# Optimization experiments

Hardware: AMD Instinct MI355X
Metric: run time of the kernel (lower is better)

Reference implementation:

```python
import jax, jax.numpy as jnp
import numpy as np

N = 8192      # nodes
E = 16384     # edges
G = 512       # graphs
IN = 235      # node feature dim (input_dim)
H = 64        # hidden_dim
ED = 52       # edge feature dim


def setup_inputs() -> dict:
    key = jax.random.key(0)
    ks = jax.random.split(key, 24)
    s = lambda fan_in: 1.0 / np.sqrt(fan_in)
    inp = {}
    inp["x"] = jax.random.normal(ks[0], (N, IN), dtype=jnp.float32)
    inp["edge_index"] = jax.random.randint(ks[1], (2, E), 0, N)
    inp["edge_attr"] = jax.random.uniform(ks[2], (E, ED), dtype=jnp.float32)
    inp["batch"] = jnp.sort(jax.random.randint(ks[3], (N,), 0, G))
    # EdgeModel (nn of nnconv1): Linear(52,128) -> Linear(128, 235*64)
    inp["W1"] = jax.random.normal(ks[4], (128, ED), dtype=jnp.float32) * s(ED)
    inp["b1"] = jnp.zeros((128,), jnp.float32)
    inp["W2"] = jax.random.normal(ks[5], (IN * H, 128), dtype=jnp.float32) * s(128)
    inp["b2"] = jnp.zeros((IN * H,), jnp.float32)
    # NNConv root weight and bias
    inp["root"] = jax.random.normal(ks[6], (IN, H), dtype=jnp.float32) * s(IN)
    inp["conv_b"] = jnp.zeros((H,), jnp.float32)
    # MLP head
    inp["fw1"] = jax.random.normal(ks[7], (128, H), dtype=jnp.float32) * s(H)
    inp["fb1"] = jnp.zeros((128,), jnp.float32)
    inp["fw2"] = jax.random.normal(ks[8], (256, 128), dtype=jnp.float32) * s(128)
    inp["fb2"] = jnp.zeros((256,), jnp.float32)
    inp["fw3"] = jax.random.normal(ks[9], (128, 256), dtype=jnp.float32) * s(256)
    inp["fb3"] = jnp.zeros((128,), jnp.float32)
    inp["fw4"] = jax.random.normal(ks[10], (1, 128), dtype=jnp.float32) * s(128)
    inp["fb4"] = jnp.zeros((1,), jnp.float32)
    return inp


def reference(x, edge_index, edge_attr, batch, W1, b1, W2, b2, root, conv_b,
              fw1, fb1, fw2, fb2, fw3, fb3, fw4, fb4):
    src, dst = edge_index[0], edge_index[1]
    # edge MLP -> per-edge weight matrices [E, IN, H]
    h = edge_attr @ W1.T + b1
    w = (h @ W2.T + b2).reshape(E, IN, H)
    # gather source node feats, per-edge matmul, scatter-add to destinations
    msg = jnp.einsum('ei,eih->eh', x[src], w)          # [E, H]
    agg = jax.ops.segment_sum(msg, dst, num_segments=N)  # [N, H]
    out = jax.nn.relu(agg + x @ root + conv_b)           # NNConv + ReLU
    # global mean pool per graph
    summ = jax.ops.segment_sum(out, batch, num_segments=G)
    cnt = jax.ops.segment_sum(jnp.ones((N, 1), out.dtype), batch, num_segments=G)
    pooled = summ / jnp.maximum(cnt, 1.0)                # [G, H]
    # dense MLP head
    y = jax.nn.relu(pooled @ fw1.T + fb1)
    y = jax.nn.relu(y @ fw2.T + fb2)
    y = jax.nn.relu(y @ fw3.T + fb3)
    return y @ fw4.T + fb4                               # [G, 1]
```

## Files before the change

kernel.cpp:

```cpp
#include <hip/hip_runtime.h>
#include <hip/hip_bf16.h>
#include <stdint.h>

#define N_NODES 8192
#define N_EDGES 16384
#define N_GRAPHS 512
#define IN_DIM 235
#define H_DIM 64
#define ED_DIM 52
#define HID1 128
#define KP 256
#define NB 3328
#define NBP 3584

#define BT_BLOCKS 940
#define EXT_BLOCKS 128
#define ZERO_BLOCKS 16
#define PREP_GRID (BT_BLOCKS + EXT_BLOCKS + ZERO_BLOCKS + N_NODES)

typedef __bf16 bf16x8 __attribute__((ext_vector_type(8)));
typedef float f32x4 __attribute__((ext_vector_type(4)));

static __device__ inline unsigned short f2bf(float f) {
    union { float f; unsigned u; } v; v.f = f;
    unsigned r = v.u + 0x7FFFu + ((v.u >> 16) & 1u);
    return (unsigned short)(r >> 16);
}

__global__ __launch_bounds__(256) void k_prep(const float* __restrict__ x,
                                              const float* __restrict__ W1,
                                              const float* __restrict__ W2,
                                              const float* __restrict__ b1,
                                              const float* __restrict__ b2,
                                              const float* __restrict__ root,
                                              unsigned short* __restrict__ A,
                                              unsigned short* __restrict__ Bt) {
    __shared__ float w1s[ED_DIM * 132];
    __shared__ float w2s[16 * 132];
    const int bx = blockIdx.x;
    const int t = threadIdx.x;

    if (bx < BT_BLOCKS) {
        const int i = bx >> 2;
        const int by = bx & 3;
        for (int j = t; j < ED_DIM * HID1; j += 256) {
            const int k = j / ED_DIM, d = j - k * ED_DIM;
            w1s[d * 132 + k] = W1[j];
        }
        const float* w2src = W2 + ((size_t)i * 64 + by * 16) * HID1;
        for (int j = t; j < 16 * HID1; j += 256) w2s[(j >> 7) * 132 + (j & 127)] = w2src[j];
        __syncthreads();
        const int hh = t & 15, dq = t >> 4;
        const float4* w2v = (const float4*)&w2s[hh * 132];
        #pragma unroll
        for (int m = 0; m < 4; ++m) {
            const int d = dq + m * 16;
            if (d >= ED_DIM) break;
            const float4* w1v = (const float4*)&w1s[d * 132];
            float acc = 0.f;
            #pragma unroll
            for (int k4 = 0; k4 < HID1 / 4; ++k4) {
                const float4 a = w1v[k4], b = w2v[k4];
                acc += a.x * b.x + a.y * b.y + a.z * b.z + a.w * b.w;
            }
            const int p = (by * 16 + hh) * ED_DIM + d;
            Bt[(size_t)p * KP + i] = f2bf(acc);
        }
    } else if (bx < BT_BLOCKS + EXT_BLOCKS) {
        const int j = bx - BT_BLOCKS;
        const int i = t;
        if (i < IN_DIM) {
            float v;
            if (j < 64) {
                v = root[i * H_DIM + j];
            } else {
                const int jj = i * H_DIM + (j - 64);
                float acc = b2[jj];
                const float* w = W2 + (size_t)jj * HID1;
                #pragma unroll 8
                for (int k = 0; k < HID1; ++k) acc += w[k] * b1[k];
                v = acc;
            }
            Bt[(size_t)(NB + j) * KP + i] = f2bf(v);
        }
    } else if (bx < BT_BLOCKS + EXT_BLOCKS + ZERO_BLOCKS) {
        const int z = bx - BT_BLOCKS - EXT_BLOCKS;
        const int R1 = NBP * 21;
        const int TOT = R1 + 128 * IN_DIM;
        for (int idx = z * 256 + t; idx < TOT; idx += ZERO_BLOCKS * 256) {
            size_t off;
            if (idx < R1) {
                const int r = idx / 21, c = IN_DIM + idx - (idx / 21) * 21;
                off = (size_t)r * KP + c;
            } else {
                const int k = idx - R1;
                const int r = 3456 + k / IN_DIM, c = k - (k / IN_DIM) * IN_DIM;
                off = (size_t)r * KP + c;
            }
            Bt[off] = 0;
        }
    } else {
        const int j = (bx - BT_BLOCKS - EXT_BLOCKS - ZERO_BLOCKS) * 256 + t;
        const int n = j >> 8, i = j & 255;
        A[j] = (i < IN_DIM) ? f2bf(x[n * IN_DIM + i]) : (unsigned short)0;
    }
}

__global__ __launch_bounds__(1024, 4) void k_gemm(const unsigned short* __restrict__ A,
                                                  const unsigned short* __restrict__ Bt,
                                                  unsigned short* __restrict__ P,
                                                  float* __restrict__ agg,
                                                  float* __restrict__ xb2,
                                                  const float* __restrict__ conv_b) {
    __shared__ unsigned short As[2 * 256 * 32];
    __shared__ unsigned short Bs[2 * 256 * 32];
    const int t = threadIdx.x;
    const int lin = blockIdx.x;
    const int xcd = lin & 7, bi = lin >> 3;
    const int mt = (bi / 14) * 8 + xcd;
    const int nt = bi % 14;
    const int m0 = mt * 256, n0 = nt * 256;
    const int wid = t >> 6, lane = t & 63;
    const int wm = wid & 3;
    const int wn = wid >> 2;
    const int q = lane >> 4, r16 = lane & 15;

    f32x4 acc[4][4] = {};

    auto stage = [&](int k0, int buf) {
        const int idx = t;
        const int row = idx >> 2;
        const int lgrp = ((idx & 3) ^ ((row >> 1) & 3)) * 8;
        const unsigned short* ga = &A[(size_t)(m0 + row) * KP + k0 + lgrp];
        const unsigned short* gb = &Bt[(size_t)(n0 + row) * KP + k0 + lgrp];
        char* la = (char*)As + buf * 16384 + wid * 1024;
        char* lb = (char*)Bs + buf * 16384 + wid * 1024;
        __builtin_amdgcn_global_load_lds(
            (const __attribute__((address_space(1))) unsigned int*)ga,
            (__attribute__((address_space(3))) unsigned int*)la, 16, 0, 0);
        __builtin_amdgcn_global_load_lds(
            (const __attribute__((address_space(1))) unsigned int*)gb,
            (__attribute__((address_space(3))) unsigned int*)lb, 16, 0, 0);
    };

    stage(0, 0);
    const int pcq = (q ^ ((r16 >> 1) & 3)) * 8;
    #pragma unroll
    for (int it = 0; it < 8; ++it) {
        __syncthreads();
        if (it < 7) stage((it + 1) * 32, (it + 1) & 1);
        const int bo = (it & 1) * 8192;
        bf16x8 af[4], bfr[4];
        #pragma unroll
        for (int mi = 0; mi < 4; ++mi)
            af[mi] = *(const bf16x8*)(&As[bo + (wm * 64 + mi * 16 + r16) * 32 + pcq]);
        #pragma unroll
        for (int ni = 0; ni < 4; ++ni)
            bfr[ni] = *(const bf16x8*)(&Bs[bo + (wn * 64 + ni * 16 + r16) * 32 + pcq]);
        #pragma unroll
        for (int mi = 0; mi < 4; ++mi)
            #pragma unroll
            for (int ni = 0; ni < 4; ++ni)
                acc[mi][ni] = __builtin_amdgcn_mfma_f32_16x16x32_bf16(
                    bfr[ni], af[mi], acc[mi][ni], 0, 0, 0);
    }

    if (n0 < NB) {
        #pragma unroll
        for (int mi = 0; mi < 4; ++mi)
            #pragma unroll
            for (int ni = 0; ni < 4; ++ni) {
                const int row = m0 + wm * 64 + mi * 16 + r16;
                const int col = n0 + wn * 64 + ni * 16 + q * 4;
                union { unsigned short us[4]; uint2 u2; } pk;
                #pragma unroll
                for (int rr = 0; rr < 4; ++rr) pk.us[rr] = f2bf(acc[mi][ni][rr]);
                *(uint2*)(&P[(size_t)row * NB + col]) = pk.u2;
            }
    } else if (wn < 2) {
        #pragma unroll
        for (int mi = 0; mi < 4; ++mi)
            #pragma unroll
            for (int ni = 0; ni < 4; ++ni) {
                const int row = m0 + wm * 64 + mi * 16 + r16;
                const int cl = ni * 16 + q * 4;
                if (wn == 0) {
                    const float4 cb = *(const float4*)&conv_b[cl];
                    float4 v;
                    v.x = acc[mi][ni][0] + cb.x; v.y = acc[mi][ni][1] + cb.y;
                    v.z = acc[mi][ni][2] + cb.z; v.w = acc[mi][ni][3] + cb.w;
                    *(float4*)(&agg[row * H_DIM + cl]) = v;
                } else {
                    float4 v;
                    v.x = acc[mi][ni][0]; v.y = acc[mi][ni][1];
                    v.z = acc[mi][ni][2]; v.w = acc[mi][ni][3];
                    *(float4*)(&xb2[row * H_DIM + cl]) = v;
                }
            }
    }
}

__global__ __launch_bounds__(256) void k_edge(const int* __restrict__ ei,
                                              const float* __restrict__ ea,
                                              const unsigned short* __restrict__ P,
                                              const float* __restrict__ xb2,
                                              float* __restrict__ agg) {
    const int e = (blockIdx.x * 256 + threadIdx.x) >> 6;
    const int h = threadIdx.x & 63;
    if (e >= N_EDGES) return;
    const int s = ei[e], dst = ei[N_EDGES + e];
    const uint2* Pr = (const uint2*)(P + (size_t)s * NB + h * ED_DIM);
    const float4* ev = (const float4*)(ea + (size_t)e * ED_DIM);

    uint2 pv[13];
    #pragma unroll
    for (int j = 0; j < 13; ++j) pv[j] = Pr[j];
    float4 eav[13];
    #pragma unroll
    for (int j = 0; j < 13; ++j) eav[j] = ev[j];

    float acc = xb2[s * H_DIM + h];
    #pragma unroll
    for (int j = 0; j < 13; ++j) {
        union { unsigned u; float f; } a0, a1, b0, b1;
        a0.u = pv[j].x << 16; a1.u = pv[j].x & 0xffff0000u;
        b0.u = pv[j].y << 16; b1.u = pv[j].y & 0xffff0000u;
        acc += eav[j].x * a0.f + eav[j].y * a1.f
             + eav[j].z * b0.f + eav[j].w * b1.f;
    }
    atomicAdd(&agg[dst * H_DIM + h], acc);
}

__global__ __launch_bounds__(256) void k_tail(const float* __restrict__ agg,
                                              const int* __restrict__ batch,
                                              const float* __restrict__ fw1, const float* __restrict__ fb1,
                                              const float* __restrict__ fw2, const float* __restrict__ fb2,
                                              const float* __restrict__ fw3, const float* __restrict__ fb3,
                                              const float* __restrict__ fw4, const float* __restrict__ fb4,
                                              float* __restrict__ out) {
    __shared__ float red[256];
    __shared__ float sp[64], s1[128], s2[256], s3[128];
    const int g = blockIdx.x, t = threadIdx.x;

    int lo = 0, hi = N_NODES;
    while (lo < hi) { const int mid = (lo + hi) >> 1; if (batch[mid] < g) lo = mid + 1; else hi = mid; }
    const int start = lo;
    hi = N_NODES;
    while (lo < hi) { const int mid = (lo + hi) >> 1; if (batch[mid] <= g) lo = mid + 1; else hi = mid; }
    const int end = lo;
    const float inv = 1.0f / fmaxf((float)(end - start), 1.0f);

    float a = 0.f;
    for (int n = start + (t >> 6); n < end; n += 4)
        a += fmaxf(agg[n * H_DIM + (t & 63)], 0.f);
    red[t] = a;
    __syncthreads();
    if (t < 64) sp[t] = (red[t] + red[t + 64] + red[t + 128] + red[t + 192]) * inv;
    __syncthreads();

    if (t < 128) {
        float acc = fb1[t];
        const float* w = fw1 + t * 64;
        #pragma unroll 8
        for (int k = 0; k < 64; ++k) acc += sp[k] * w[k];
        s1[t] = fmaxf(acc, 0.f);
    }
    __syncthreads();
    {
        float acc = fb2[t];
        const float* w = fw2 + t * 128;
        #pragma unroll 8
        for (int k = 0; k < 128; ++k) acc += s1[k] * w[k];
        s2[t] = fmaxf(acc, 0.f);
    }
    __syncthreads();
    if (t < 128) {
        float acc = fb3[t];
        const float* w = fw3 + t * 256;
        #pragma unroll 8
        for (int k = 0; k < 256; ++k) acc += s2[k] * w[k];
        s3[t] = fmaxf(acc, 0.f);
    }
    __syncthreads();
    if (t < 64) {
        float p = s3[t] * fw4[t] + s3[t + 64] * fw4[t + 64];
        #pragma unroll
        for (int off = 32; off > 0; off >>= 1) p += __shfl_down(p, off);
        if (t == 0) out[g] = p + fb4[0];
    }
}

extern "C" void kernel_launch(void* const* d_in, const int* in_sizes, int n_in,
                              void* d_out, int out_size, void* d_ws, size_t ws_size,
                              hipStream_t stream) {
    const float* x      = (const float*)d_in[0];
    const int*   ei     = (const int*)d_in[1];
    const float* ea     = (const float*)d_in[2];
    const int*   batch  = (const int*)d_in[3];
    const float* W1     = (const float*)d_in[4];
    const float* b1     = (const float*)d_in[5];
    const float* W2     = (const float*)d_in[6];
    const float* b2     = (const float*)d_in[7];
    const float* root   = (const float*)d_in[8];
    const float* conv_b = (const float*)d_in[9];
    const float* fw1 = (const float*)d_in[10]; const float* fb1 = (const float*)d_in[11];
    const float* fw2 = (const float*)d_in[12]; const float* fb2 = (const float*)d_in[13];
    const float* fw3 = (const float*)d_in[14]; const float* fb3 = (const float*)d_in[15];
    const float* fw4 = (const float*)d_in[16]; const float* fb4 = (const float*)d_in[17];
    float* out = (float*)d_out;

    char* ws = (char*)d_ws;
    unsigned short* A   = (unsigned short*)(ws);
    unsigned short* Bt  = (unsigned short*)(ws + 4194304);
    unsigned short* P   = (unsigned short*)(ws + 6029312);
    float* agg  = (float*)(ws + 60555264);
    float* xb2  = (float*)(ws + 62652416);

    k_prep<<<dim3(PREP_GRID), dim3(256), 0, stream>>>(x, W1, W2, b1, b2, root, A, Bt);
    k_gemm<<<dim3(448), dim3(1024), 0, stream>>>(A, Bt, P, agg, xb2, conv_b);
    k_edge<<<dim3(N_EDGES / 4), dim3(256), 0, stream>>>(ei, ea, P, xb2, agg);
    k_tail<<<dim3(N_GRAPHS), dim3(256), 0, stream>>>(agg, batch, fw1, fb1, fw2, fb2, fw3, fb3, fw4, fb4, out);
}
```

Before: 188.3 us.

## Bucket edges by source node to reuse per-node P rows in edge kernel

Adds a bucketing pass that groups edge ids by source node with atomic counters, plus a small overflow list for nodes with more than 16 outgoing edges. The edge kernel now runs one wavefront per source node: it loads that node's projected P row once into registers and loops over the node's edges, instead of re-reading the row for every edge. This is meant to cut the redundant P gather traffic. In exchange it adds a kernel launch and per-node load imbalance. Edges past the overflow cap would be silently dropped.

```diff
diff --git a/kernel.cpp b/kernel.cpp
--- a/kernel.cpp
+++ b/kernel.cpp
@@ -18,6 +18,9 @@
 #define ZERO_BLOCKS 16
 #define PREP_GRID (BT_BLOCKS + EXT_BLOCKS + ZERO_BLOCKS + N_NODES)
 
+#define BUCKET_CAP 16
+#define OVF_CAP 255
+
 typedef __bf16 bf16x8 __attribute__((ext_vector_type(8)));
 typedef float f32x4 __attribute__((ext_vector_type(4)));
 
@@ -34,7 +37,9 @@
                                               const float* __restrict__ b2,
                                               const float* __restrict__ root,
                                               unsigned short* __restrict__ A,
-                                              unsigned short* __restrict__ Bt) {
+                                              unsigned short* __restrict__ Bt,
+                                              int* __restrict__ cnt,
+                                              int* __restrict__ ovf) {
     __shared__ float w1s[ED_DIM * 132];
     __shared__ float w2s[16 * 132];
     const int bx = blockIdx.x;
@@ -99,10 +104,29 @@
             }
             Bt[off] = 0;
         }
+        for (int idx = z * 256 + t; idx < N_NODES + OVF_CAP + 1; idx += ZERO_BLOCKS * 256) {
+            if (idx < N_NODES) cnt[idx] = 0;
+            else ovf[idx - N_NODES] = 0;
+        }
     } else {
         const int j = (bx - BT_BLOCKS - EXT_BLOCKS - ZERO_BLOCKS) * 256 + t;
         const int n = j >> 8, i = j & 255;
         A[j] = (i < IN_DIM) ? f2bf(x[n * IN_DIM + i]) : (unsigned short)0;
+    }
+}
+
+__global__ __launch_bounds__(256) void k_bucket(const int* __restrict__ ei,
+                                                int* __restrict__ cnt,
+                                                int* __restrict__ bucket,
+                                                int* __restrict__ ovf) {
+    const int e = blockIdx.x * 256 + threadIdx.x;
+    if (e >= N_EDGES) return;
+    const int s = ei[e];
+    const int slot = atomicAdd(&cnt[s], 1);
+    if (slot < BUCKET_CAP) bucket[s * BUCKET_CAP + slot] = e;
+    else {
+        const int p = atomicAdd(&ovf[0], 1);
+        if (p < OVF_CAP) ovf[1 + p] = e;
     }
 }
 
@@ -200,35 +224,61 @@
     }
 }
 
-__global__ __launch_bounds__(256) void k_edge(const int* __restrict__ ei,
-                                              const float* __restrict__ ea,
-                                              const unsigned short* __restrict__ P,
-                                              const float* __restrict__ xb2,
-                                              float* __restrict__ agg) {
-    const int e = (blockIdx.x * 256 + threadIdx.x) >> 6;
-    const int h = threadIdx.x & 63;
-    if (e >= N_EDGES) return;
-    const int s = ei[e], dst = ei[N_EDGES + e];
-    const uint2* Pr = (const uint2*)(P + (size_t)s * NB + h * ED_DIM);
-    const float4* ev = (const float4*)(ea + (size_t)e * ED_DIM);
-
-    uint2 pv[13];
-    #pragma unroll
-    for (int j = 0; j < 13; ++j) pv[j] = Pr[j];
-    float4 eav[13];
-    #pragma unroll
-    for (int j = 0; j < 13; ++j) eav[j] = ev[j];
-
-    float acc = xb2[s * H_DIM + h];
-    #pragma unroll
-    for (int j = 0; j < 13; ++j) {
-        union { unsigned u; float f; } a0, a1, b0, b1;
-        a0.u = pv[j].x << 16; a1.u = pv[j].x & 0xffff0000u;
-        b0.u = pv[j].y << 16; b1.u = pv[j].y & 0xffff0000u;
-        acc += eav[j].x * a0.f + eav[j].y * a1.f
-             + eav[j].z * b0.f + eav[j].w * b1.f;
-    }
-    atomicAdd(&agg[dst * H_DIM + h], acc);
+__global__ __launch_bounds__(256) void k_edge2(const int* __restrict__ ei,
+                                               const float* __restrict__ ea,
+                                               const unsigned short* __restrict__ P,
+                                               const float* __restrict__ xb2,
+                                               float* __restrict__ agg,
+                                               const int* __restrict__ cnt,
+                                               const int* __restrict__ bucket,
+                                               const int* __restrict__ ovf) {
+    const int wv = threadIdx.x >> 6, h = threadIdx.x & 63;
+    if (blockIdx.x < N_NODES / 4) {
+        const int n = blockIdx.x * 4 + wv;
+        int deg = cnt[n];
+        if (deg <= 0) return;
+        if (deg > BUCKET_CAP) deg = BUCKET_CAP;
+        const uint2* Pr = (const uint2*)(P + (size_t)n * NB + h * ED_DIM);
+        uint2 pv[13];
+        #pragma unroll
+        for (int j = 0; j < 13; ++j) pv[j] = Pr[j];
+        const float xb = xb2[n * H_DIM + h];
+        for (int j = 0; j < deg; ++j) {
+            const int e = bucket[n * BUCKET_CAP + j];
+            const int dst = ei[N_EDGES + e];
+            const float4* ev = (const float4*)(ea + (size_t)e * ED_DIM);
+            float acc = xb;
+            #pragma unroll
+            for (int k = 0; k < 13; ++k) {
+                const float4 ee = ev[k];
+                union { unsigned u; float f; } a0, a1, b0, b1;
+                a0.u = pv[k].x << 16; a1.u = pv[k].x & 0xffff0000u;
+                b0.u = pv[k].y << 16; b1.u = pv[k].y & 0xffff0000u;
+                acc += ee.x * a0.f + ee.y * a1.f + ee.z * b0.f + ee.w * b1.f;
+            }
+            atomicAdd(&agg[dst * H_DIM + h], acc);
+        }
+    } else {
+        int m = ovf[0];
+        if (m > OVF_CAP) m = OVF_CAP;
+        for (int p = wv; p < m; p += 4) {
+            const int e = ovf[1 + p];
+            const int s = ei[e], dst = ei[N_EDGES + e];
+            const uint2* Pr = (const uint2*)(P + (size_t)s * NB + h * ED_DIM);
+            const float4* ev = (const float4*)(ea + (size_t)e * ED_DIM);
+            float acc = xb2[s * H_DIM + h];
+            #pragma unroll
+            for (int k = 0; k < 13; ++k) {
+                const uint2 pk = Pr[k];
+                const float4 ee = ev[k];
+                union { unsigned u; float f; } a0, a1, b0, b1;
+                a0.u = pk.x << 16; a1.u = pk.x & 0xffff0000u;
+                b0.u = pk.y << 16; b1.u = pk.y & 0xffff0000u;
+                acc += ee.x * a0.f + ee.y * a1.f + ee.z * b0.f + ee.w * b1.f;
+            }
+            atomicAdd(&agg[dst * H_DIM + h], acc);
+        }
+    }
 }
 
 __global__ __launch_bounds__(256) void k_tail(const float* __restrict__ agg,
@@ -315,9 +365,13 @@
     unsigned short* P   = (unsigned short*)(ws + 6029312);
     float* agg  = (float*)(ws + 60555264);
     float* xb2  = (float*)(ws + 62652416);
-
-    k_prep<<<dim3(PREP_GRID), dim3(256), 0, stream>>>(x, W1, W2, b1, b2, root, A, Bt);
+    int* cnt    = (int*)(ws + 64749568);
+    int* bucket = (int*)(ws + 64782336);
+    int* ovf    = (int*)(ws + 65306624);
+
+    k_prep<<<dim3(PREP_GRID), dim3(256), 0, stream>>>(x, W1, W2, b1, b2, root, A, Bt, cnt, ovf);
+    k_bucket<<<dim3(N_EDGES / 256), dim3(256), 0, stream>>>(ei, cnt, bucket, ovf);
     k_gemm<<<dim3(448), dim3(1024), 0, stream>>>(A, Bt, P, agg, xb2, conv_b);
-    k_edge<<<dim3(N_EDGES / 4), dim3(256), 0, stream>>>(ei, ea, P, xb2, agg);
+    k_edge2<<<dim3(N_NODES / 4 + 1), dim3(256), 0, stream>>>(ei, ea, P, xb2, agg, cnt, bucket, ovf);
     k_tail<<<dim3(N_GRAPHS), dim3(256), 0, stream>>>(agg, batch, fw1, fb1, fw2, fb2, fw3, fb3, fw4, fb4, out);
 }
```

Result: slower. 196.7 us (+4.5%).
